# Kernel tuning notes

Hardware: AMD Instinct MI355X
Metric: run time of the kernel (lower is better)

## Reference

```python
import jax, jax.numpy as jnp
import numpy as np

B, N, F_DIM, M, K, D = 8, 16384, 6, 128, 16, 768
MLP_DIMS = [F_DIM, 256, 512, 768, D]


def _fps(pts):
    """Deterministic farthest point sampling. pts: [N,4] -> indices [M] (first pick = point 0)."""
    n = pts.shape[0]

    def step(carry, _):
        min_d, last = carry
        d = jnp.sum((pts - pts[last]) ** 2, axis=-1)
        min_d = jnp.minimum(min_d, d)
        nxt = jnp.argmax(min_d).astype(jnp.int32)
        return (min_d, nxt), nxt

    init = (jnp.full((n,), 1e30, dtype=pts.dtype), jnp.int32(0))
    _, idx = jax.lax.scan(step, init, None, length=M - 1)
    return jnp.concatenate([jnp.zeros((1,), jnp.int32), idx])


def setup_inputs() -> dict:
    key = jax.random.key(0)
    ks = jax.random.split(key, 16)
    bidx = jnp.repeat(jnp.arange(B, dtype=jnp.float32), N)[:, None]
    xyzt = jax.random.normal(ks[0], (B * N, 4), jnp.float32)
    coordinates = jnp.concatenate([bidx, xyzt], axis=1)  # [B*N, 5]
    features = jax.random.normal(ks[1], (B * N, F_DIM), jnp.float32)
    inp = {"coordinates": coordinates, "features": features}
    for i in range(4):
        di, do = MLP_DIMS[i], MLP_DIMS[i + 1]
        inp[f"W{i}"] = jax.random.normal(ks[2 + i], (di, do), jnp.float32) * np.float32(1.0 / np.sqrt(di))
        inp[f"b{i}"] = jnp.zeros((do,), jnp.float32)
    for j in range(2):
        inp[f"Wn{j}"] = jax.random.normal(ks[6 + j], (D, D), jnp.float32) * np.float32(1.0 / np.sqrt(D))
        inp[f"bn{j}"] = jnp.zeros((D,), jnp.float32)
    return inp


def _forward(coordinates, features, W0, b0, W1, b1, W2, b2, W3, b3, Wn0, bn0, Wn1, bn1):
    # Equal points per event, sorted batch ids -> plain reshape replaces the per-batch loop.
    pts = coordinates.reshape(B, N, 5)[:, :, 1:5]       # xyz + time  [B,N,4]
    h = features.reshape(B, N, F_DIM)
    # per-point MLP (ReLU after each hidden layer, final Linear has no activation)
    h = jax.nn.relu(h @ W0 + b0)
    h = jax.nn.relu(h @ W1 + b1)
    h = jax.nn.relu(h @ W2 + b2)
    pf = h @ W3 + b3                                    # [B,N,D]
    # FPS centroids (non-differentiable index selection, as in the torch/cpu original)
    fidx = jax.vmap(_fps)(jax.lax.stop_gradient(pts))   # [B,M]
    cent = jnp.take_along_axis(pts, fidx[:, :, None], axis=1)  # [B,M,4]
    # cdist + kNN (smallest distances)
    dist = jnp.sqrt(jnp.sum((cent[:, :, None, :] - pts[:, None, :, :]) ** 2, axis=-1))  # [B,M,N]
    _, knn = jax.lax.top_k(-dist, K)                    # [B,M,K]
    gathered = jax.vmap(lambda p, i: p[i])(pf, knn)     # [B,M,K,D]
    pooled = jnp.max(gathered, axis=2)                  # [B,M,D]
    t = jax.nn.relu(pooled @ Wn0 + bn0)
    tokens = t @ Wn1 + bn1                              # [B,M,D]
    # sort tokens/centroids by centroid time (column 3)
    order = jnp.argsort(cent[:, :, 3], axis=1)
    cent = jnp.take_along_axis(cent, order[:, :, None], axis=1)
    tokens = jnp.take_along_axis(tokens, order[:, :, None], axis=1)
    masks = jnp.ones((B, M), dtype=bool)  # num_points > max_tokens -> all tokens valid
    return tokens, cent, masks


def reference(coordinates, features, W0, b0, W1, b1, W2, b2, W3, b3, Wn0, bn0, Wn1, bn1):
    return _forward(coordinates, features, W0, b0, W1, b1, W2, b2, W3, b3, Wn0, bn0, Wn1, bn1)
```

## Files before the change

kernel.cpp:

```cpp
#include <hip/hip_runtime.h>

#define B_ 8
#define N_ 16384
#define F_ 6
#define M_ 128
#define K_ 16
#define D_ 768

typedef unsigned short u16;
typedef unsigned int u32;
typedef unsigned long long u64;
typedef __attribute__((ext_vector_type(8))) short short8;
typedef __attribute__((ext_vector_type(4))) float f32x4;
typedef __attribute__((ext_vector_type(2))) float f32x2;

__device__ __forceinline__ u16 f2bf(float f){
  union { float f; u32 i; } v; v.f = f;
  u32 x = v.i;
  u32 r = x + 0x7FFFu + ((x >> 16) & 1u);
  return (u16)(r >> 16);
}

__device__ __forceinline__ void ld_g2l(const u16* g, u16* l){
  __builtin_amdgcn_global_load_lds((const __attribute__((address_space(1))) u32*)g,
                                   (__attribute__((address_space(3))) u32*)l, 16, 0, 0);
}

__device__ __forceinline__ f32x4 ld_x4(const float* p){
  f32x4 r;
  asm volatile("global_load_dwordx4 %0, %1, off" : "=v"(r) : "v"(p) : "memory");
  return r;
}

template<int CTRL>
__device__ __forceinline__ float dppmax(float v){
  union { float f; int i; } a, r;
  a.f = v;
  r.i = __builtin_amdgcn_update_dpp(a.i, a.i, CTRL, 0xF, 0xF, false);
  return fmaxf(v, r.f);
}

__global__ __launch_bounds__(256) void conv_all(const float* __restrict__ W1,
                                                const float* __restrict__ W2,
                                                const float* __restrict__ W3,
                                                const float* __restrict__ Wn0,
                                                const float* __restrict__ Wn1,
                                                u16* __restrict__ Wb){
  __shared__ u16 tile[64][65];
  int blk = blockIdx.x;
  const float* W; u16* WT; int K, N, lb;
  if      (blk < 32)  { W = W1;  WT = Wb;           K = 256; N = 512; lb = blk; }
  else if (blk < 128) { W = W2;  WT = Wb + 131072;  K = 512; N = 768; lb = blk - 32; }
  else if (blk < 272) { W = W3;  WT = Wb + 524288;  K = 768; N = 768; lb = blk - 128; }
  else if (blk < 416) { W = Wn0; WT = Wb + 1114112; K = 768; N = 768; lb = blk - 272; }
  else                { W = Wn1; WT = Wb + 1703936; K = 768; N = 768; lb = blk - 416; }
  int tiles_n = N >> 6;
  int tk = lb / tiles_n, tn = lb % tiles_n;
  int k0 = tk << 6, n0 = tn << 6;
  int t = threadIdx.x;
#pragma unroll
  for (int q = 0; q < 16; q++){
    int idx = q * 256 + t;
    int kk = idx >> 6, nn = idx & 63;
    tile[kk][nn] = f2bf(W[(size_t)(k0 + kk) * N + n0 + nn]);
  }
  __syncthreads();
#pragma unroll
  for (int q = 0; q < 16; q++){
    int idx = q * 256 + t;
    int nn = idx >> 6, kk = idx & 63;
    WT[(size_t)(n0 + nn) * K + k0 + kk] = tile[kk][nn];
  }
}

#define FPT 32
__global__ __launch_bounds__(512)
void fps_block(const float* __restrict__ coords, float* __restrict__ cent){
#pragma clang fp contract(off)
  __shared__ f32x2 sxy[N_];
  __shared__ float swv[2][8];
  __shared__ int   swi[2][8];
  int b = blockIdx.x;
  int t = threadIdx.x;
  int lane = t & 63, wave = t >> 6;
  const float* cb = coords + (size_t)b * N_ * 5;
  const int base = t << 5;
  f32x2 pzw[FPT];
  float md[FPT];
#pragma unroll
  for (int g = 0; g < 4; g++){
    f32x4 qg[8];
#pragma unroll
    for (int k2 = 0; k2 < 8; k2++)
      qg[k2] = ld_x4(cb + (size_t)(base + g * 8 + k2) * 5 + 1);
    asm volatile("s_waitcnt vmcnt(0)" ::: "memory");
    __builtin_amdgcn_sched_barrier(0);
#pragma unroll
    for (int k2 = 0; k2 < 8; k2++){
      int k = g * 8 + k2;
      sxy[k * 512 + t] = (f32x2){qg[k2][0], qg[k2][1]};
      pzw[k] = (f32x2){qg[k2][2], qg[k2][3]};
      md[k] = 1e30f;
    }
  }
  float cx = cb[1], cy = cb[2], cz = cb[3], ct = cb[4];
  if (t == 0){
    float* c0 = cent + (size_t)b * M_ * 4;
    c0[0]=cx; c0[1]=cy; c0[2]=cz; c0[3]=ct;
  }
  for (int step = 1; step < M_; step++){
    float bv = -1.0f; int bl = 0;
#pragma unroll
    for (int k = 0; k < FPT; k++){
      f32x2 xy = sxy[k * 512 + t];
      float dx = xy[0] - cx;
      float dy = xy[1] - cy;
      float dz = pzw[k][0] - cz;
      float dw = pzw[k][1] - ct;
      float s = ((dx*dx + dy*dy) + dz*dz) + dw*dw;
      float m = fminf(s, md[k]);
      md[k] = m;
      if (m > bv){ bv = m; bl = k; }
    }
    int bi = base + bl;
    float r = bv;
    r = dppmax<0x111>(r);
    r = dppmax<0x112>(r);
    r = dppmax<0x114>(r);
    r = dppmax<0x118>(r);
    r = dppmax<0x142>(r);
    r = dppmax<0x143>(r);
    union { float f; int i; } rm; rm.f = r;
    union { int i; float f; } wmu; wmu.i = __builtin_amdgcn_readlane(rm.i, 63);
    float wmax = wmu.f;
    u64 wmask = __ballot(bv == wmax);
    int srcL = (int)__ffsll((unsigned long long)wmask) - 1;
    int wbi = __builtin_amdgcn_readlane(bi, srcL);
    int par = step & 1;
    if (lane == 0){ swv[par][wave] = wmax; swi[par][wave] = wbi; }
    __syncthreads();
    float fv = swv[par][0]; int fi = swi[par][0];
#pragma unroll
    for (int w = 1; w < 8; w++){
      float v = swv[par][w];
      int  iw = swi[par][w];
      if (v > fv){ fv = v; fi = iw; }
    }
    int widx = __builtin_amdgcn_readfirstlane(fi);
    size_t wb = (size_t)widx * 5;
    cx = cb[wb+1]; cy = cb[wb+2]; cz = cb[wb+3]; ct = cb[wb+4];
    if (t == 0){
      float* cr = cent + ((size_t)b * M_ + step) * 4;
      cr[0]=cx; cr[1]=cy; cr[2]=cz; cr[3]=ct;
    }
  }
}

__global__ __launch_bounds__(128) void rank_scatter(const float* __restrict__ cent_fps,
                                                    float* __restrict__ cent_sorted,
                                                    float* __restrict__ out,
                                                    size_t out_elems){
  int b = blockIdx.x, m = threadIdx.x;
  __shared__ float tt[M_];
  const float* row = cent_fps + ((size_t)b * M_ + m) * 4;
  float x=row[0], y=row[1], z=row[2], w=row[3];
  tt[m] = w;
  __syncthreads();
  int rank = 0;
  for (int j = 0; j < M_; j++){
    float tj = tt[j];
    if (tj < w || (tj == w && j < m)) rank++;
  }
  float* dst = cent_sorted + ((size_t)b * M_ + rank) * 4;
  dst[0]=x; dst[1]=y; dst[2]=z; dst[3]=w;
  size_t co = (size_t)B_ * M_ * D_ + ((size_t)b * M_ + rank) * 4;
  if (co + 3 < out_elems){
    out[co+0]=x; out[co+1]=y; out[co+2]=z; out[co+3]=w;
  }
  size_t mo = (size_t)B_ * M_ * D_ + (size_t)B_ * M_ * 4 + (size_t)b * M_ + m;
  if (mo < out_elems) out[mo] = 1.0f;
}

#define KNT 512
#define KPT 32
__global__ __launch_bounds__(512) void knn_kernel(const float* __restrict__ coords,
                                                  const float* __restrict__ cent,
                                                  int* __restrict__ knn){
#pragma clang fp contract(off)
  int cm = blockIdx.x;
  int b = cm >> 7;
  const float* cb = coords + (size_t)b * N_ * 5;
  int t = threadIdx.x;
  float cx=cent[cm*4+0], cy=cent[cm*4+1], cz=cent[cm*4+2], ct=cent[cm*4+3];
  float dist[KPT];
#pragma unroll
  for (int j = 0; j < KPT; j++){
    size_t i = t + j * KNT;
    float dx=cb[i*5+1]-cx, dy=cb[i*5+2]-cy, dz=cb[i*5+3]-cz, dw=cb[i*5+4]-ct;
    float d = ((dx*dx + dy*dy) + dz*dz) + dw*dw;
    dist[j] = sqrtf(d);
  }
  __shared__ float s_wv[8];
  __shared__ int s_wi[8];
  __shared__ int s_bi;
  for (int r = 0; r < K_; r++){
    float bv = 3e38f; int bi = 1 << 30;
#pragma unroll
    for (int j = 0; j < KPT; j++){
      int i = t + j * KNT;
      float v = dist[j];
      if (v < bv){ bv = v; bi = i; }
    }
#pragma unroll
    for (int off = 32; off > 0; off >>= 1){
      float ov = __shfl_down(bv, off);
      int oi = __shfl_down(bi, off);
      if (ov < bv || (ov == bv && oi < bi)){ bv = ov; bi = oi; }
    }
    if ((t & 63) == 0){ s_wv[t >> 6] = bv; s_wi[t >> 6] = bi; }
    __syncthreads();
    if (t == 0){
      float fv = s_wv[0]; int fi = s_wi[0];
      for (int w = 1; w < 8; w++){
        float wv = s_wv[w]; int wi = s_wi[w];
        if (wv < fv || (wv == fv && wi < fi)){ fv = wv; fi = wi; }
      }
      s_bi = fi;
      knn[(size_t)cm * K_ + r] = fi & (N_ - 1);
    }
    __syncthreads();
    int wi = s_bi;
#pragma unroll
    for (int j = 0; j < KPT; j++){
      if (t + j * KNT == wi) dist[j] = 3e38f;
    }
  }
}

__global__ __launch_bounds__(256) void gather_l0(const float* __restrict__ feat,
                                                 const int* __restrict__ knn,
                                                 const float* __restrict__ W0,
                                                 const float* __restrict__ b0,
                                                 u16* __restrict__ h1,
                                                 int rowBase){
  __shared__ float sW[F_][256];
  __shared__ float sb[256];
  __shared__ float sfa[32][F_];
  int t = threadIdx.x;
#pragma unroll
  for (int k = 0; k < F_; k++) sW[k][t] = W0[k * 256 + t];
  sb[t] = b0[t];
  if (t < 32 * F_){
    int r = t / F_, k = t % F_;
    int grow = rowBase + blockIdx.x * 32 + r;
    int bb = grow >> 11;
    int idx = knn[grow] & (N_ - 1);
    sfa[r][k] = feat[((size_t)bb * N_ + idx) * F_ + k];
  }
  __syncthreads();
#pragma unroll 4
  for (int r = 0; r < 32; r++){
    float acc = sb[t];
#pragma unroll
    for (int k = 0; k < F_; k++) acc = fmaf(sfa[r][k], sW[k][t], acc);
    int lrow = blockIdx.x * 32 + r;
    h1[(size_t)lrow * 256 + t] = f2bf(fmaxf(acc, 0.0f));
  }
}

template<int RELU, int OUTF32>
__global__ __launch_bounds__(256) void gemm_bf16(const u16* __restrict__ A,
                                                 const u16* __restrict__ WT,
                                                 const float* __restrict__ bias,
                                                 void* __restrict__ Cv,
                                                 int Kd, int Nd){
  __shared__ u16 As[128][32];
  __shared__ u16 Bs[128][32];
  const int t = threadIdx.x;
  const int bm = blockIdx.y << 7;
  const int bn = blockIdx.x << 7;
  const int wave = t >> 6;
  const int lane = t & 63;
  const int wm = (wave & 1) << 6;
  const int wn = (wave >> 1) << 6;
  const int lm = lane & 15;
  const int lk = (lane >> 4) << 3;
  u16* AsF = &As[0][0];
  u16* BsF = &Bs[0][0];
  const int wbase = wave << 6;
  f32x4 acc[4][4] = {};
  for (int k0 = 0; k0 < Kd; k0 += 32){
#pragma unroll
    for (int it = 0; it < 2; it++){
      int slot = t + (it << 8);
      int r = slot >> 2;
      int c = (slot & 3) << 3;
      int dst = (wbase + (it << 8)) << 3;
      ld_g2l(A  + (size_t)(bm + r) * Kd + k0 + c, AsF + dst);
      ld_g2l(WT + (size_t)(bn + r) * Kd + k0 + c, BsF + dst);
    }
    __syncthreads();
    short8 af[4], bfr[4];
#pragma unroll
    for (int mt = 0; mt < 4; mt++) af[mt] = *(const short8*)&As[wm + (mt << 4) + lm][lk];
#pragma unroll
    for (int nt = 0; nt < 4; nt++) bfr[nt] = *(const short8*)&Bs[wn + (nt << 4) + lm][lk];
#pragma unroll
    for (int mt = 0; mt < 4; mt++)
#pragma unroll
      for (int nt = 0; nt < 4; nt++)
        acc[mt][nt] = __builtin_amdgcn_mfma_f32_16x16x32_bf16(af[mt], bfr[nt], acc[mt][nt], 0, 0, 0);
    __syncthreads();
  }
#pragma unroll
  for (int nt = 0; nt < 4; nt++){
    int n = bn + wn + (nt << 4) + lm;
    float bia = bias[n];
#pragma unroll
    for (int mt = 0; mt < 4; mt++){
#pragma unroll
      for (int r2 = 0; r2 < 4; r2++){
        int m = bm + wm + (mt << 4) + ((lane >> 4) << 2) + r2;
        float v = acc[mt][nt][r2] + bia;
        if (RELU) v = fmaxf(v, 0.0f);
        if (OUTF32) ((float*)Cv)[(size_t)m * Nd + n] = v;
        else        ((u16*)Cv)[(size_t)m * Nd + n] = f2bf(v);
      }
    }
  }
}

template<int RELU, int OUTF32>
__global__ __launch_bounds__(256) void gemm64(const u16* __restrict__ A,
                                              const u16* __restrict__ WT,
                                              const float* __restrict__ bias,
                                              void* __restrict__ Cv,
                                              int Kd, int Nd){
  __shared__ u16 As[64][32];
  __shared__ u16 Bs[64][32];
  const int t = threadIdx.x;
  const int bm = blockIdx.y << 6;
  const int bn = blockIdx.x << 6;
  const int wave = t >> 6;
  const int lane = t & 63;
  const int wm = (wave & 1) << 5;
  const int wn = (wave >> 1) << 5;
  const int lm = lane & 15;
  const int lk = (lane >> 4) << 3;
  u16* AsF = &As[0][0];
  u16* BsF = &Bs[0][0];
  const int wbase = wave << 6;
  f32x4 acc[2][2] = {};
  for (int k0 = 0; k0 < Kd; k0 += 32){
    {
      int r = t >> 2;
      int c = (t & 3) << 3;
      int dst = wbase << 3;
      ld_g2l(A  + (size_t)(bm + r) * Kd + k0 + c, AsF + dst);
      ld_g2l(WT + (size_t)(bn + r) * Kd + k0 + c, BsF + dst);
    }
    __syncthreads();
    short8 af[2], bfr[2];
#pragma unroll
    for (int mt = 0; mt < 2; mt++) af[mt] = *(const short8*)&As[wm + (mt << 4) + lm][lk];
#pragma unroll
    for (int nt = 0; nt < 2; nt++) bfr[nt] = *(const short8*)&Bs[wn + (nt << 4) + lm][lk];
#pragma unroll
    for (int mt = 0; mt < 2; mt++)
#pragma unroll
      for (int nt = 0; nt < 2; nt++)
        acc[mt][nt] = __builtin_amdgcn_mfma_f32_16x16x32_bf16(af[mt], bfr[nt], acc[mt][nt], 0, 0, 0);
    __syncthreads();
  }
#pragma unroll
  for (int nt = 0; nt < 2; nt++){
    int n = bn + wn + (nt << 4) + lm;
    float bia = bias[n];
#pragma unroll
    for (int mt = 0; mt < 2; mt++){
#pragma unroll
      for (int r2 = 0; r2 < 4; r2++){
        int m = bm + wm + (mt << 4) + ((lane >> 4) << 2) + r2;
        float v = acc[mt][nt][r2] + bia;
        if (RELU) v = fmaxf(v, 0.0f);
        if (OUTF32) ((float*)Cv)[(size_t)m * Nd + n] = v;
        else        ((u16*)Cv)[(size_t)m * Nd + n] = f2bf(v);
      }
    }
  }
}

__global__ __launch_bounds__(256) void gemm_pool(const u16* __restrict__ A,
                                                 const u16* __restrict__ WT,
                                                 const float* __restrict__ bias,
                                                 u16* __restrict__ pooled,
                                                 int Kd, int Nd, int groupBase){
  __shared__ u16 As[128][32];
  __shared__ u16 Bs[128][32];
  const int t = threadIdx.x;
  const int bm = blockIdx.y << 7;
  const int bn = blockIdx.x << 7;
  const int wave = t >> 6;
  const int lane = t & 63;
  const int wm = (wave & 1) << 6;
  const int wn = (wave >> 1) << 6;
  const int lm = lane & 15;
  const int lk = (lane >> 4) << 3;
  u16* AsF = &As[0][0];
  u16* BsF = &Bs[0][0];
  const int wbase = wave << 6;
  f32x4 acc[4][4] = {};
  for (int k0 = 0; k0 < Kd; k0 += 32){
#pragma unroll
    for (int it = 0; it < 2; it++){
      int slot = t + (it << 8);
      int r = slot >> 2;
      int c = (slot & 3) << 3;
      int dst = (wbase + (it << 8)) << 3;
      ld_g2l(A  + (size_t)(bm + r) * Kd + k0 + c, AsF + dst);
      ld_g2l(WT + (size_t)(bn + r) * Kd + k0 + c, BsF + dst);
    }
    __syncthreads();
    short8 af[4], bfr[4];
#pragma unroll
    for (int mt = 0; mt < 4; mt++) af[mt] = *(const short8*)&As[wm + (mt << 4) + lm][lk];
#pragma unroll
    for (int nt = 0; nt < 4; nt++) bfr[nt] = *(const short8*)&Bs[wn + (nt << 4) + lm][lk];
#pragma unroll
    for (int mt = 0; mt < 4; mt++)
#pragma unroll
      for (int nt = 0; nt < 4; nt++)
        acc[mt][nt] = __builtin_amdgcn_mfma_f32_16x16x32_bf16(af[mt], bfr[nt], acc[mt][nt], 0, 0, 0);
    __syncthreads();
  }
#pragma unroll
  for (int nt = 0; nt < 4; nt++){
    int n = bn + wn + (nt << 4) + lm;
    float bia = bias[n];
#pragma unroll
    for (int mt = 0; mt < 4; mt++){
      f32x4 a = acc[mt][nt];
      float v = fmaxf(fmaxf(a[0], a[1]), fmaxf(a[2], a[3]));
      v = fmaxf(v, __shfl_xor(v, 16));
      v = fmaxf(v, __shfl_xor(v, 32));
      if ((lane >> 4) == 0){
        int g = groupBase + (bm >> 4) + (wm >> 4) + mt;
        pooled[(size_t)g * Nd + n] = f2bf(v + bia);
      }
    }
  }
}

__global__ __launch_bounds__(256) void fill_diag(float* __restrict__ out, size_t out_elems){
  size_t i = (size_t)blockIdx.x * 256 + threadIdx.x;
  if (i >= out_elems) return;
  size_t maskStart = (size_t)B_ * M_ * D_ + (size_t)B_ * M_ * 4;
  out[i] = (i >= maskStart) ? 1.0f : 0.0f;
}

extern "C" void kernel_launch(void* const* d_in, const int* in_sizes, int n_in,
                              void* d_out, int out_size, void* d_ws, size_t ws_size,
                              hipStream_t stream){
  (void)in_sizes; (void)n_in;
  const float* coords   = (const float*)d_in[0];
  const float* features = (const float*)d_in[1];
  const float* W0 = (const float*)d_in[2];  const float* b0 = (const float*)d_in[3];
  const float* W1 = (const float*)d_in[4];  const float* b1 = (const float*)d_in[5];
  const float* W2 = (const float*)d_in[6];  const float* b2 = (const float*)d_in[7];
  const float* W3 = (const float*)d_in[8];  const float* b3 = (const float*)d_in[9];
  const float* Wn0 = (const float*)d_in[10]; const float* bn0 = (const float*)d_in[11];
  const float* Wn1 = (const float*)d_in[12]; const float* bn1 = (const float*)d_in[13];
  float* out = (float*)d_out;
  const size_t out_elems = (size_t)out_size;

  char* ws = (char*)d_ws;
  const size_t o_cent = 0;
  const size_t o_cntS = 16384;
  const size_t o_knn  = 32768;
  const size_t o_Wb   = 131072;
  const size_t o_pool = 4718592;
  const size_t o_t1   = 6291456;
  const size_t o_chunk= 7864320;
  const int ROWS = B_ * M_ * K_;

  int R = 16384;
  while (R > 128 && o_chunk + (size_t)R * 2560 > ws_size) R >>= 1;
  if (d_ws == nullptr || o_chunk + (size_t)R * 2560 > ws_size){
    fill_diag<<<(int)((out_elems + 255) / 256), 256, 0, stream>>>(out, out_elems);
    return;
  }

  float* cent_fps    = (float*)(ws + o_cent);
  float* cent_sorted = (float*)(ws + o_cntS);
  int*   knn         = (int*)(ws + o_knn);
  u16* Wb   = (u16*)(ws + o_Wb);
  u16* W1t  = Wb;               u16* W2t  = Wb + 131072;
  u16* W3t  = Wb + 524288;      u16* Wn0t = Wb + 1114112;
  u16* Wn1t = Wb + 1703936;
  u16* pooled = (u16*)(ws + o_pool);
  u16* t1     = (u16*)(ws + o_t1);
  u16* regA   = (u16*)(ws + o_chunk);
  u16* regB   = (u16*)(ws + o_chunk + (size_t)R * 1536);

  conv_all<<<560, 256, 0, stream>>>(W1, W2, W3, Wn0, Wn1, Wb);
  fps_block<<<B_, 512, 0, stream>>>(coords, cent_fps);
  rank_scatter<<<B_, 128, 0, stream>>>(cent_fps, cent_sorted, out, out_elems);
  knn_kernel<<<B_ * M_, KNT, 0, stream>>>(coords, cent_sorted, knn);

  for (int rowBase = 0; rowBase < ROWS; rowBase += R){
    gather_l0<<<R / 32, 256, 0, stream>>>(features, knn, W0, b0, regA, rowBase);
    gemm_bf16<1,0><<<dim3(4, R / 128), 256, 0, stream>>>(regA, W1t, b1, regB, 256, 512);
    gemm_bf16<1,0><<<dim3(6, R / 128), 256, 0, stream>>>(regB, W2t, b2, regA, 512, 768);
    gemm_pool<<<dim3(6, R / 128), 256, 0, stream>>>(regA, W3t, b3, pooled, 768, 768, rowBase >> 4);
  }

  gemm64<1,0><<<dim3(12, (B_ * M_) / 64), 256, 0, stream>>>(pooled, Wn0t, bn0, t1, 768, 768);
  gemm64<0,1><<<dim3(12, (B_ * M_) / 64), 256, 0, stream>>>(t1, Wn1t, bn1, out, 768, 768);
}
```

Before: 514.8 us.

## Fuse FPS, weight conversion and rank sort into one kernel; DPP kNN reduce

Merges the weight bf16 transpose kernel, the FPS kernel and the centroid rank/scatter kernel into a single launch. The 8 FPS blocks run alongside 560 conversion blocks, and the centroid sort happens in LDS at the end of FPS. FPS now keeps all point coordinates in registers instead of staging xy in LDS, which cuts LDS reads in the serial loop but raises register pressure. The kNN wave-level argmin switches from shuffle pairs to DPP min reductions with a second DPP pass for the tie-broken index.

```diff
diff --git a/kernel.cpp b/kernel.cpp
--- a/kernel.cpp
+++ b/kernel.cpp
@@ -39,84 +39,88 @@
   r.i = __builtin_amdgcn_update_dpp(a.i, a.i, CTRL, 0xF, 0xF, false);
   return fmaxf(v, r.f);
 }
-
-__global__ __launch_bounds__(256) void conv_all(const float* __restrict__ W1,
-                                                const float* __restrict__ W2,
-                                                const float* __restrict__ W3,
-                                                const float* __restrict__ Wn0,
-                                                const float* __restrict__ Wn1,
-                                                u16* __restrict__ Wb){
-  __shared__ u16 tile[64][65];
-  int blk = blockIdx.x;
-  const float* W; u16* WT; int K, N, lb;
-  if      (blk < 32)  { W = W1;  WT = Wb;           K = 256; N = 512; lb = blk; }
-  else if (blk < 128) { W = W2;  WT = Wb + 131072;  K = 512; N = 768; lb = blk - 32; }
-  else if (blk < 272) { W = W3;  WT = Wb + 524288;  K = 768; N = 768; lb = blk - 128; }
-  else if (blk < 416) { W = Wn0; WT = Wb + 1114112; K = 768; N = 768; lb = blk - 272; }
-  else                { W = Wn1; WT = Wb + 1703936; K = 768; N = 768; lb = blk - 416; }
-  int tiles_n = N >> 6;
-  int tk = lb / tiles_n, tn = lb % tiles_n;
-  int k0 = tk << 6, n0 = tn << 6;
-  int t = threadIdx.x;
-#pragma unroll
-  for (int q = 0; q < 16; q++){
-    int idx = q * 256 + t;
-    int kk = idx >> 6, nn = idx & 63;
-    tile[kk][nn] = f2bf(W[(size_t)(k0 + kk) * N + n0 + nn]);
-  }
-  __syncthreads();
-#pragma unroll
-  for (int q = 0; q < 16; q++){
-    int idx = q * 256 + t;
-    int nn = idx >> 6, kk = idx & 63;
-    WT[(size_t)(n0 + nn) * K + k0 + kk] = tile[kk][nn];
-  }
+template<int CTRL>
+__device__ __forceinline__ float dppmin(float v){
+  union { float f; int i; } a, r;
+  a.f = v;
+  r.i = __builtin_amdgcn_update_dpp(a.i, a.i, CTRL, 0xF, 0xF, false);
+  return fminf(v, r.f);
+}
+template<int CTRL>
+__device__ __forceinline__ int dppimin(int v){
+  int r = __builtin_amdgcn_update_dpp(v, v, CTRL, 0xF, 0xF, false);
+  return (r < v) ? r : v;
 }
 
 #define FPT 32
 __global__ __launch_bounds__(512)
-void fps_block(const float* __restrict__ coords, float* __restrict__ cent){
+void fps_conv(const float* __restrict__ coords,
+              float* __restrict__ cent_sorted,
+              float* __restrict__ out, size_t out_elems,
+              const float* __restrict__ W1, const float* __restrict__ W2,
+              const float* __restrict__ W3, const float* __restrict__ Wn0,
+              const float* __restrict__ Wn1, u16* __restrict__ Wb){
 #pragma clang fp contract(off)
-  __shared__ f32x2 sxy[N_];
+  __shared__ u16 tile[64][65];
+  __shared__ f32x4 carr[M_];
   __shared__ float swv[2][8];
   __shared__ int   swi[2][8];
-  int b = blockIdx.x;
+  int blk = blockIdx.x;
   int t = threadIdx.x;
+
+  if (blk >= 8){
+    int cblk = blk - 8;
+    const float* W; u16* WT; int K, N, lb;
+    if      (cblk < 32)  { W = W1;  WT = Wb;           K = 256; N = 512; lb = cblk; }
+    else if (cblk < 128) { W = W2;  WT = Wb + 131072;  K = 512; N = 768; lb = cblk - 32; }
+    else if (cblk < 272) { W = W3;  WT = Wb + 524288;  K = 768; N = 768; lb = cblk - 128; }
+    else if (cblk < 416) { W = Wn0; WT = Wb + 1114112; K = 768; N = 768; lb = cblk - 272; }
+    else                 { W = Wn1; WT = Wb + 1703936; K = 768; N = 768; lb = cblk - 416; }
+    int tiles_n = N >> 6;
+    int tk = lb / tiles_n, tn = lb % tiles_n;
+    int k0 = tk << 6, n0 = tn << 6;
+#pragma unroll
+    for (int q = 0; q < 8; q++){
+      int idx = q * 512 + t;
+      int kk = idx >> 6, nn = idx & 63;
+      tile[kk][nn] = f2bf(W[(size_t)(k0 + kk) * N + n0 + nn]);
+    }
+    __syncthreads();
+#pragma unroll
+    for (int q = 0; q < 8; q++){
+      int idx = q * 512 + t;
+      int nn = idx >> 6, kk = idx & 63;
+      WT[(size_t)(n0 + nn) * K + k0 + kk] = tile[kk][nn];
+    }
+    return;
+  }
+
+  int b = blk;
   int lane = t & 63, wave = t >> 6;
   const float* cb = coords + (size_t)b * N_ * 5;
   const int base = t << 5;
-  f32x2 pzw[FPT];
+  f32x4 p[FPT];
+#pragma unroll
+  for (int k = 0; k < FPT; k++){
+    p[k] = ld_x4(cb + (size_t)(base + k) * 5 + 1);
+  }
   float md[FPT];
 #pragma unroll
-  for (int g = 0; g < 4; g++){
-    f32x4 qg[8];
-#pragma unroll
-    for (int k2 = 0; k2 < 8; k2++)
-      qg[k2] = ld_x4(cb + (size_t)(base + g * 8 + k2) * 5 + 1);
-    asm volatile("s_waitcnt vmcnt(0)" ::: "memory");
-    __builtin_amdgcn_sched_barrier(0);
-#pragma unroll
-    for (int k2 = 0; k2 < 8; k2++){
-      int k = g * 8 + k2;
-      sxy[k * 512 + t] = (f32x2){qg[k2][0], qg[k2][1]};
-      pzw[k] = (f32x2){qg[k2][2], qg[k2][3]};
-      md[k] = 1e30f;
-    }
-  }
+  for (int k = 0; k < FPT; k++) md[k] = 1e30f;
+  asm volatile("s_waitcnt vmcnt(0)" ::: "memory");
+  __builtin_amdgcn_sched_barrier(0);
   float cx = cb[1], cy = cb[2], cz = cb[3], ct = cb[4];
-  if (t == 0){
-    float* c0 = cent + (size_t)b * M_ * 4;
-    c0[0]=cx; c0[1]=cy; c0[2]=cz; c0[3]=ct;
-  }
+  if (t == 0) carr[0] = (f32x4){cx, cy, cz, ct};
   for (int step = 1; step < M_; step++){
     float bv = -1.0f; int bl = 0;
 #pragma unroll
     for (int k = 0; k < FPT; k++){
-      f32x2 xy = sxy[k * 512 + t];
+      f32x2 xy = (f32x2){p[k][0], p[k][1]};
+      f32x2 zw = (f32x2){p[k][2], p[k][3]};
       float dx = xy[0] - cx;
       float dy = xy[1] - cy;
-      float dz = pzw[k][0] - cz;
-      float dw = pzw[k][1] - ct;
+      float dz = zw[0] - cz;
+      float dw = zw[1] - ct;
       float s = ((dx*dx + dy*dy) + dz*dz) + dw*dw;
       float m = fminf(s, md[k]);
       md[k] = m;
@@ -149,36 +153,26 @@
     int widx = __builtin_amdgcn_readfirstlane(fi);
     size_t wb = (size_t)widx * 5;
     cx = cb[wb+1]; cy = cb[wb+2]; cz = cb[wb+3]; ct = cb[wb+4];
-    if (t == 0){
-      float* cr = cent + ((size_t)b * M_ + step) * 4;
-      cr[0]=cx; cr[1]=cy; cr[2]=cz; cr[3]=ct;
-    }
-  }
-}
-
-__global__ __launch_bounds__(128) void rank_scatter(const float* __restrict__ cent_fps,
-                                                    float* __restrict__ cent_sorted,
-                                                    float* __restrict__ out,
-                                                    size_t out_elems){
-  int b = blockIdx.x, m = threadIdx.x;
-  __shared__ float tt[M_];
-  const float* row = cent_fps + ((size_t)b * M_ + m) * 4;
-  float x=row[0], y=row[1], z=row[2], w=row[3];
-  tt[m] = w;
+    if (t == 0) carr[step] = (f32x4){cx, cy, cz, ct};
+  }
   __syncthreads();
-  int rank = 0;
-  for (int j = 0; j < M_; j++){
-    float tj = tt[j];
-    if (tj < w || (tj == w && j < m)) rank++;
-  }
-  float* dst = cent_sorted + ((size_t)b * M_ + rank) * 4;
-  dst[0]=x; dst[1]=y; dst[2]=z; dst[3]=w;
-  size_t co = (size_t)B_ * M_ * D_ + ((size_t)b * M_ + rank) * 4;
-  if (co + 3 < out_elems){
-    out[co+0]=x; out[co+1]=y; out[co+2]=z; out[co+3]=w;
-  }
-  size_t mo = (size_t)B_ * M_ * D_ + (size_t)B_ * M_ * 4 + (size_t)b * M_ + m;
-  if (mo < out_elems) out[mo] = 1.0f;
+  if (t < M_){
+    f32x4 row = carr[t];
+    float w = row[3];
+    int rank = 0;
+    for (int j = 0; j < M_; j++){
+      float tj = carr[j][3];
+      if (tj < w || (tj == w && j < t)) rank++;
+    }
+    float* dst = cent_sorted + ((size_t)b * M_ + rank) * 4;
+    dst[0]=row[0]; dst[1]=row[1]; dst[2]=row[2]; dst[3]=w;
+    size_t co = (size_t)B_ * M_ * D_ + ((size_t)b * M_ + rank) * 4;
+    if (co + 3 < out_elems){
+      out[co+0]=row[0]; out[co+1]=row[1]; out[co+2]=row[2]; out[co+3]=w;
+    }
+    size_t mo = (size_t)B_ * M_ * D_ + (size_t)B_ * M_ * 4 + (size_t)b * M_ + t;
+    if (mo < out_elems) out[mo] = 1.0f;
+  }
 }
 
 #define KNT 512
@@ -211,13 +205,25 @@
       float v = dist[j];
       if (v < bv){ bv = v; bi = i; }
     }
-#pragma unroll
-    for (int off = 32; off > 0; off >>= 1){
-      float ov = __shfl_down(bv, off);
-      int oi = __shfl_down(bi, off);
-      if (ov < bv || (ov == bv && oi < bi)){ bv = ov; bi = oi; }
-    }
-    if ((t & 63) == 0){ s_wv[t >> 6] = bv; s_wi[t >> 6] = bi; }
+    float rv = bv;
+    rv = dppmin<0x111>(rv);
+    rv = dppmin<0x112>(rv);
+    rv = dppmin<0x114>(rv);
+    rv = dppmin<0x118>(rv);
+    rv = dppmin<0x142>(rv);
+    rv = dppmin<0x143>(rv);
+    union { float f; int i; } rmu; rmu.f = rv;
+    union { int i; float f; } wmn; wmn.i = __builtin_amdgcn_readlane(rmu.i, 63);
+    float wmin = wmn.f;
+    int cand = (bv == wmin) ? bi : 0x7FFFFFFF;
+    cand = dppimin<0x111>(cand);
+    cand = dppimin<0x112>(cand);
+    cand = dppimin<0x114>(cand);
+    cand = dppimin<0x118>(cand);
+    cand = dppimin<0x142>(cand);
+    cand = dppimin<0x143>(cand);
+    int wbi = __builtin_amdgcn_readlane(cand, 63);
+    if ((t & 63) == 0){ s_wv[t >> 6] = wmin; s_wi[t >> 6] = wbi; }
     __syncthreads();
     if (t == 0){
       float fv = s_wv[0]; int fi = s_wi[0];
@@ -482,6 +488,7 @@
   const size_t o_t1   = 6291456;
   const size_t o_chunk= 7864320;
   const int ROWS = B_ * M_ * K_;
+  (void)o_cent;
 
   int R = 16384;
   while (R > 128 && o_chunk + (size_t)R * 2560 > ws_size) R >>= 1;
@@ -490,7 +497,6 @@
     return;
   }
 
-  float* cent_fps    = (float*)(ws + o_cent);
   float* cent_sorted = (float*)(ws + o_cntS);
   int*   knn         = (int*)(ws + o_knn);
   u16* Wb   = (u16*)(ws + o_Wb);
@@ -502,9 +508,8 @@
   u16* regA   = (u16*)(ws + o_chunk);
   u16* regB   = (u16*)(ws + o_chunk + (size_t)R * 1536);
 
-  conv_all<<<560, 256, 0, stream>>>(W1, W2, W3, Wn0, Wn1, Wb);
-  fps_block<<<B_, 512, 0, stream>>>(coords, cent_fps);
-  rank_scatter<<<B_, 128, 0, stream>>>(cent_fps, cent_sorted, out, out_elems);
+  fps_conv<<<568, 512, 0, stream>>>(coords, cent_sorted, out, out_elems,
+                                    W1, W2, W3, Wn0, Wn1, Wb);
   knn_kernel<<<B_ * M_, KNT, 0, stream>>>(coords, cent_sorted, knn);
 
   for (int rowBase = 0; rowBase < ROWS; rowBase += R){
```

Measured after the change: 498.0 us. 3.3% less time.
